# Performance work log

Hardware: AMD Instinct MI355X
Metric: run time of the kernel (lower is better)

Reference implementation:

```python
import jax, jax.numpy as jnp
from jax import lax
import numpy as np

B, C, H, W = 8, 64, 56, 56
LM = 9              # level_map: NSCT subbands per channel
D = LM * C + C      # 640: swin block dim
DEPTH = 2
WIN = 7
HEADS = 8
KS = 5              # NSCT filter kernel size


def _nsct_filters():
    # fixed nonsubsampled 9-band filter bank (lowpass + 8 directional), stand-in for myNSCTd
    r = np.arange(KS) - KS // 2
    yy, xx = np.meshgrid(r, r, indexing='ij')
    g = np.exp(-(xx ** 2 + yy ** 2) / 4.0)
    g = g / g.sum()
    f = [g]
    for k in range(LM - 1):
        th = k * np.pi / (LM - 1)
        d = (np.cos(th) * xx + np.sin(th) * yy) * g
        d = d - d.mean()
        d = d / np.sqrt((d ** 2).sum())
        f.append(d)
    return jnp.asarray(np.stack(f), dtype=jnp.float32)  # [LM,KS,KS]


def _ct(x):
    # per-(b,c) NSCT decomposition -> [B, LM*C, H, W], band-major (matches transpose(0,2,1,3,4).reshape)
    Bx, Cx, Hx, Wx = x.shape
    K = _nsct_filters()
    k = jnp.tile(K, (Cx, 1, 1))[:, None]  # [Cx*LM,1,KS,KS], out channel index c*LM+band
    o = lax.conv_general_dilated(x, k, (1, 1), 'SAME',
                                 dimension_numbers=('NCHW', 'OIHW', 'NCHW'),
                                 feature_group_count=Cx)
    o = o.reshape(Bx, Cx, LM, Hx, Wx).transpose(0, 2, 1, 3, 4).reshape(Bx, LM * Cx, Hx, Wx)
    return o


def _ict(y):
    # inverse transform: reshape(B,LM,C,H,W).permute(0,2,1,3,4), reconstruct per channel
    Bx = y.shape[0]
    t = y.reshape(Bx, LM, C, H, W).transpose(0, 2, 1, 3, 4).reshape(Bx, C * LM, H, W)
    K = _nsct_filters()
    g = jnp.broadcast_to(K, (C, LM, KS, KS))  # groups=C: 9 subbands -> 1 channel each
    return lax.conv_general_dilated(t, g, (1, 1), 'SAME',
                                    dimension_numbers=('NCHW', 'OIHW', 'NCHW'),
                                    feature_group_count=C)


def _ln(x, g, b):
    m = x.mean(-1, keepdims=True)
    v = x.var(-1, keepdims=True)
    return (x - m) / jnp.sqrt(v + 1e-5) * g + b


def _attn_mask(shift):
    # standard SW-MSA mask for shifted windows
    img = np.zeros((H, W), np.int32)
    c = 0
    for hs in (slice(0, -WIN), slice(-WIN, -shift), slice(-shift, None)):
        for ws in (slice(0, -WIN), slice(-WIN, -shift), slice(-shift, None)):
            img[hs, ws] = c
            c += 1
    a = img.reshape(H // WIN, WIN, W // WIN, WIN).transpose(0, 2, 1, 3).reshape(-1, WIN * WIN)
    m = np.where(a[:, :, None] != a[:, None, :], -1e9, 0.0).astype(np.float32)
    return jnp.asarray(m)  # [nWindows, T, T]


def _swin_block(x, p, shift):
    Bx = x.shape[0]
    T = WIN * WIN
    dh = D // HEADS
    nH, nWw = H // WIN, W // WIN
    sc = x
    h = _ln(x, p['ln1_g'], p['ln1_b'])
    if shift:
        h = jnp.roll(h, (-shift, -shift), (1, 2))
    w = h.reshape(Bx, nH, WIN, nWw, WIN, D).transpose(0, 1, 3, 2, 4, 5).reshape(Bx * nH * nWw, T, D)
    qkv = w @ p['qkv_w'] + p['qkv_b']
    q, k, v = jnp.split(qkv, 3, axis=-1)
    heads = lambda t: t.reshape(-1, T, HEADS, dh).transpose(0, 2, 1, 3)
    q, k, v = heads(q), heads(k), heads(v)
    s = jnp.einsum('nhtd,nhsd->nhts', q, k) / jnp.sqrt(jnp.asarray(dh, x.dtype))
    if shift:
        m = _attn_mask(shift)
        s = (s.reshape(Bx, nH * nWw, HEADS, T, T) + m[None, :, None]).reshape(-1, HEADS, T, T)
    a = jax.nn.softmax(s, -1)
    o = jnp.einsum('nhts,nhsd->nhtd', a, v).transpose(0, 2, 1, 3).reshape(-1, T, D)
    o = o @ p['proj_w'] + p['proj_b']
    o = o.reshape(Bx, nH, nWw, WIN, WIN, D).transpose(0, 1, 3, 2, 4, 5).reshape(Bx, H, W, D)
    if shift:
        o = jnp.roll(o, (shift, shift), (1, 2))
    x = sc + o
    h2 = _ln(x, p['ln2_g'], p['ln2_b'])
    h2 = jax.nn.gelu(h2 @ p['fc1_w'] + p['fc1_b']) @ p['fc2_w'] + p['fc2_b']
    return x + h2


def setup_inputs() -> dict:
    key = jax.random.key(0)
    ks = jax.random.split(key, 8)
    s = 0.02
    n = lambda k, shp: jax.random.normal(k, shp, jnp.float32) * s
    return {
        'x': jax.random.normal(ks[0], (B, C, H, W), jnp.float32),
        'ln1_g': jnp.ones((DEPTH, D), jnp.float32), 'ln1_b': jnp.zeros((DEPTH, D), jnp.float32),
        'qkv_w': n(ks[1], (DEPTH, D, 3 * D)), 'qkv_b': jnp.zeros((DEPTH, 3 * D), jnp.float32),
        'proj_w': n(ks[2], (DEPTH, D, D)), 'proj_b': jnp.zeros((DEPTH, D), jnp.float32),
        'ln2_g': jnp.ones((DEPTH, D), jnp.float32), 'ln2_b': jnp.zeros((DEPTH, D), jnp.float32),
        'fc1_w': n(ks[3], (DEPTH, D, 4 * D)), 'fc1_b': jnp.zeros((DEPTH, 4 * D), jnp.float32),
        'fc2_w': n(ks[4], (DEPTH, 4 * D, D)), 'fc2_b': jnp.zeros((DEPTH, D), jnp.float32),
        'lin_w': n(ks[5], (D, LM * C)), 'lin_b': jnp.zeros((LM * C,), jnp.float32),
        'conv_w': n(ks[6], (C, D)), 'conv_b': jnp.zeros((C,), jnp.float32),
    }


def reference(x, ln1_g, ln1_b, qkv_w, qkv_b, proj_w, proj_b, ln2_g, ln2_b,
              fc1_w, fc1_b, fc2_w, fc2_b, lin_w, lin_b, conv_w, conv_b):
    x2 = jax.nn.relu(x)
    x_trans = lax.stop_gradient(_ct(x2))          # CT detaches its input in the original
    x3 = jnp.concatenate([x_trans, x2], axis=1)   # [B, 10C, H, W]
    x3 = x3.transpose(0, 2, 3, 1)                 # BHWC
    for i in range(DEPTH):
        p = dict(ln1_g=ln1_g[i], ln1_b=ln1_b[i], qkv_w=qkv_w[i], qkv_b=qkv_b[i],
                 proj_w=proj_w[i], proj_b=proj_b[i], ln2_g=ln2_g[i], ln2_b=ln2_b[i],
                 fc1_w=fc1_w[i], fc1_b=fc1_b[i], fc2_w=fc2_w[i], fc2_b=fc2_b[i])
        x3 = _swin_block(x3, p, 0 if i % 2 == 0 else WIN // 2)
    x3 = x3 @ lin_w + lin_b                        # D -> LM*C
    y = x3.transpose(0, 3, 1, 2)                   # [B, 9C, H, W]
    y_trans = lax.stop_gradient(_ict(y))           # ICT detaches its input in the original
    yc = jnp.concatenate([y_trans, y], axis=1)     # [B, 10C, H, W]
    out = jnp.einsum('bchw,oc->bohw', yc, conv_w) + conv_b[None, :, None, None]
    return out
```

## Files before the change

### kernel.cpp

```cpp
#include <hip/hip_runtime.h>
#include <hip/hip_bf16.h>
#include <math.h>

typedef __attribute__((ext_vector_type(4))) float f32x4;
typedef __attribute__((ext_vector_type(8))) short short8;

#define NTOK 25088
#define DD   640

__device__ __forceinline__ void gload_lds16(const void* g, void* l) {
    __builtin_amdgcn_global_load_lds((const __attribute__((address_space(1))) void*)g,
                                     (__attribute__((address_space(3))) void*)l,
                                     16, 0, 0);
}

__device__ __forceinline__ float gelu_f(float t) {
    float u = 1.5957691216057308f * (t + 0.044715f * t * t * t);
    float e = __builtin_amdgcn_exp2f(u * -1.4426950408889634f);
    return t / (1.f + e);
}

__global__ void init_consts(float* __restrict__ filt, float* __restrict__ linbp,
                            const float* __restrict__ lin_b, float* __restrict__ convbp,
                            const float* __restrict__ conv_b) {
    int t = threadIdx.x;
    if (t == 0) {
        float g[25]; float s = 0.f;
        for (int i = 0; i < 5; i++) for (int j = 0; j < 5; j++) {
            float yy = (float)(i - 2), xx = (float)(j - 2);
            float v = expf(-(xx*xx + yy*yy) * 0.25f);
            g[i*5+j] = v; s += v;
        }
        for (int i = 0; i < 25; i++) { g[i] /= s; filt[i] = g[i]; }
        for (int k = 0; k < 8; k++) {
            float th = (float)k * 3.14159265358979323846f / 8.f;
            float ct = cosf(th), st = sinf(th);
            float d[25]; float mean = 0.f;
            for (int i = 0; i < 5; i++) for (int j = 0; j < 5; j++) {
                float yy = (float)(i - 2), xx = (float)(j - 2);
                d[i*5+j] = (ct*xx + st*yy) * g[i*5+j];
                mean += d[i*5+j];
            }
            mean *= (1.f/25.f);
            float ss = 0.f;
            for (int i = 0; i < 25; i++) { d[i] -= mean; ss += d[i]*d[i]; }
            ss = sqrtf(ss);
            for (int i = 0; i < 25; i++) filt[(k+1)*25 + i] = d[i] / ss;
        }
    }
    for (int i = t; i < 640; i += 256) linbp[i]  = (i < 576) ? lin_b[i]  : 0.f;
    for (int i = t; i < 128; i += 256) convbp[i] = (i < 64)  ? conv_b[i] : 0.f;
}

__global__ __launch_bounds__(256)
void wtrans_kernel(const float* __restrict__ src, __hip_bfloat16* __restrict__ dst,
                   int K, int Nsrc) {
    __shared__ float tile[32][33];
    const int n0 = blockIdx.x * 32;
    const int k0 = blockIdx.y * 32;
    const int tx = threadIdx.x, ty = threadIdx.y;
    #pragma unroll
    for (int r = ty; r < 32; r += 8) {
        int k = k0 + r, n = n0 + tx;
        tile[r][tx] = (n < Nsrc) ? src[(long)k * Nsrc + n] : 0.f;
    }
    __syncthreads();
    #pragma unroll
    for (int r = ty; r < 32; r += 8) {
        int n = n0 + r, k = k0 + tx;
        dst[(long)n * K + k] = __float2bfloat16(tile[tx][r]);
    }
}

__global__ void wcast_kernel(const float* __restrict__ src, __hip_bfloat16* __restrict__ dst,
                             int count, int total) {
    int i = blockIdx.x * 256 + threadIdx.x;
    if (i < total) dst[i] = __float2bfloat16(i < count ? src[i] : 0.f);
}

__global__ __launch_bounds__(256)
void prep_kernel(const float* __restrict__ x, const float* __restrict__ filt,
                 float* __restrict__ x3) {
    __shared__ float sf[225];
    for (int i = threadIdx.x; i < 225; i += 256) sf[i] = filt[i];
    __syncthreads();
    int id = blockIdx.x * 256 + threadIdx.x;
    int c = id & 63;
    int pix = id >> 6;
    int w = pix % 56, h = (pix / 56) % 56, b = pix / 3136;
    const float* xp = x + (long)(b * 64 + c) * 3136;
    float nb[25];
    #pragma unroll
    for (int dy = 0; dy < 5; dy++) {
        int hy = h + dy - 2;
        #pragma unroll
        for (int dx = 0; dx < 5; dx++) {
            int wx = w + dx - 2;
            float v = 0.f;
            if (hy >= 0 && hy < 56 && wx >= 0 && wx < 56) v = fmaxf(xp[hy*56 + wx], 0.f);
            nb[dy*5 + dx] = v;
        }
    }
    float* orow = x3 + (long)pix * DD;
    #pragma unroll
    for (int band = 0; band < 9; band++) {
        float a = 0.f;
        #pragma unroll
        for (int t = 0; t < 25; t++) a += nb[t] * sf[band*25 + t];
        orow[band*64 + c] = a;
    }
    orow[576 + c] = nb[12];
}

__global__ __launch_bounds__(256)
void ln_kernel(const float* __restrict__ xin, const float* __restrict__ g,
               const float* __restrict__ bt, __hip_bfloat16* __restrict__ out) {
    const int lane = threadIdx.x & 63;
    const long tok = (long)blockIdx.x * 4 + (threadIdx.x >> 6);
    const float* xr = xin + tok * DD;
    float v[10]; float s = 0.f, s2 = 0.f;
    #pragma unroll
    for (int i = 0; i < 10; i++) { float t = xr[lane + (i << 6)]; v[i] = t; s += t; s2 += t*t; }
    #pragma unroll
    for (int o = 32; o > 0; o >>= 1) { s += __shfl_down(s, o); s2 += __shfl_down(s2, o); }
    s = __shfl(s, 0); s2 = __shfl(s2, 0);
    const float mean = s * (1.f/640.f);
    const float var  = s2 * (1.f/640.f) - mean * mean;
    const float inv  = 1.f / sqrtf(var + 1e-5f);
    __hip_bfloat16* orow = out + tok * DD;
    #pragma unroll
    for (int i = 0; i < 10; i++) {
        int c = lane + (i << 6);
        orow[c] = __float2bfloat16((v[i] - mean) * inv * g[c] + bt[c]);
    }
}

__global__ __launch_bounds__(256, 3)
void gemm128_kernel(const __hip_bfloat16* __restrict__ A,
                    const __hip_bfloat16* __restrict__ Bt,
                    const float* __restrict__ bias,
                    const float* __restrict__ resid,
                    float* __restrict__ Cf,
                    __hip_bfloat16* __restrict__ Cb,
                    int K, int ldc, int ncf, int ldb, int col_off, int ncb,
                    int act_gelu, int nvalid, int mode) {
    extern __shared__ __align__(16) char smraw[];

    const int tid  = threadIdx.x;
    const int lane = tid & 63;
    const int wv   = tid >> 6;
    const int wr   = wv >> 1;
    const int wc   = wv & 1;

    const int gx   = gridDim.x;
    const int nwg  = gx * gridDim.y;
    const int orig = blockIdx.y * gx + blockIdx.x;
    const int qq = nwg >> 3, rr = nwg & 7;
    const int xcd = orig & 7, lid = orig >> 3;
    const int wg = (xcd < rr ? xcd * (qq + 1) : rr * (qq + 1) + (xcd - rr) * qq) + lid;
    const long m0 = (long)(wg / gx) * 128;
    const long n0 = (long)(wg % gx) * 128;

    const bool wact = ((int)n0 + (wc << 6)) < nvalid;

    f32x4 acc[4][4];
    #pragma unroll
    for (int i = 0; i < 4; i++)
        #pragma unroll
        for (int j = 0; j < 4; j++) acc[i][j] = (f32x4){0.f, 0.f, 0.f, 0.f};

    const int r0  = tid >> 2;
    const int sl  = tid & 3;
    const int ssl = sl ^ ((r0 >> 1) & 3);
    const __hip_bfloat16* Agb = A  + (m0 + r0) * (long)K + (ssl << 3);
    const __hip_bfloat16* Bgb = Bt + (n0 + r0) * (long)K + (ssl << 3);
    char* dA = smraw + r0 * 64 + sl * 16;
    char* dB = dA + 8192;

    const int frow = lane & 15;
    const int fks  = lane >> 4;
    const int colA = (fks ^ ((frow >> 1) & 3)) << 4;

    auto STAGE = [&](int b, int kt) {
        const long ko = (long)kt << 5;
        gload_lds16(Agb + ko,                dA + b * 16384);
        gload_lds16(Agb + 64 * (long)K + ko, dA + b * 16384 + 4096);
        gload_lds16(Bgb + ko,                dB + b * 16384);
        gload_lds16(Bgb + 64 * (long)K + ko, dB + b * 16384 + 4096);
    };

    const int nt = K >> 5;
    STAGE(0, 0);
    for (int t = 0; t < nt; ++t) {
        asm volatile("s_waitcnt vmcnt(0)" ::: "memory");
        __builtin_amdgcn_s_barrier();
        __builtin_amdgcn_sched_barrier(0);
        if (t + 1 < nt) STAGE((t + 1) & 1, t + 1);
        if (wact) {
            const char* pA = smraw + (t & 1) * 16384;
            const char* pB = pA + 8192;
            short8 af[4], bfr[4];
            #pragma unroll
            for (int mi = 0; mi < 4; ++mi)
                af[mi] = *(const short8*)(pA + ((wr << 6) + (mi << 4) + frow) * 64 + colA);
            #pragma unroll
            for (int nj = 0; nj < 4; ++nj)
                bfr[nj] = *(const short8*)(pB + ((wc << 6) + (nj << 4) + frow) * 64 + colA);
            __builtin_amdgcn_s_setprio(1);
            #pragma unroll
            for (int mi = 0; mi < 4; ++mi)
                #pragma unroll
                for (int nj = 0; nj < 4; ++nj)
                    acc[mi][nj] = __builtin_amdgcn_mfma_f32_16x16x32_bf16(
                        bfr[nj], af[mi], acc[mi][nj], 0, 0, 0);
            __builtin_amdgcn_s_setprio(0);
        }
    }

    if (!wact) return;
    const int nlim = (ncf > ncb) ? ncf : ncb;
    #pragma unroll
    for (int mi = 0; mi < 4; ++mi) {
        const long row = m0 + (wr << 6) + (mi << 4) + frow;
        #pragma unroll
        for (int nj = 0; nj < 4; ++nj) {
            const int n = (int)n0 + (wc << 6) + (nj << 4) + (fks << 2);
            if (n >= nlim) continue;
            f32x4 v = acc[mi][nj];
            if (bias) {
                const f32x4 bv = *(const f32x4*)&bias[n];
                v += bv;
            }
            if (act_gelu) {
                v[0] = gelu_f(v[0]); v[1] = gelu_f(v[1]); v[2] = gelu_f(v[2]); v[3] = gelu_f(v[3]);
            }
            if (mode == 1) {
                const int b = (int)(row / 3136), pos = (int)(row % 3136);
                #pragma unroll
                for (int r = 0; r < 4; ++r)
                    Cf[(long)(b * 64 + n + r) * 3136 + pos] = v[r];
                continue;
            }
            if (resid && n < ncf) v += *(const f32x4*)&resid[row * (long)ldc + n];
            if (Cf && n < ncf) *(f32x4*)&Cf[row * (long)ldc + n] = v;
            if (Cb && n < ncb) {
                short4 p;
                p.x = (short)__bfloat16_as_short(__float2bfloat16(v[0]));
                p.y = (short)__bfloat16_as_short(__float2bfloat16(v[1]));
                p.z = (short)__bfloat16_as_short(__float2bfloat16(v[2]));
                p.w = (short)__bfloat16_as_short(__float2bfloat16(v[3]));
                *(short4*)&Cb[row * (long)ldb + col_off + n] = p;
            }
        }
    }
}

__global__ __launch_bounds__(256)
void attn_kernel(const __hip_bfloat16* __restrict__ qkv, __hip_bfloat16* __restrict__ o,
                 int shift) {
    __shared__ __align__(16) float qT[80][52];
    __shared__ __align__(16) float kT[80][52];
    __shared__ __align__(16) float vs[50][80];
    __shared__ __align__(16) float ss[49][52];
    __shared__ int toks[49];
    __shared__ int rid[49];

    const int tid = threadIdx.x;
    const int win = blockIdx.x >> 3;
    const int hd  = blockIdx.x & 7;
    const int b   = win >> 6;
    const int wh  = (win >> 3) & 7;
    const int ww  = win & 7;

    if (tid < 49) {
        int i = tid / 7, j = tid % 7;
        int ph = wh * 7 + i, pw = ww * 7 + j;
        int sh = ph + shift; if (sh >= 56) sh -= 56;
        int sw = pw + shift; if (sw >= 56) sw -= 56;
        toks[tid] = (b * 56 + sh) * 56 + sw;
        int rh = (ph < 49) ? 0 : ((ph < 53) ? 1 : 2);
        int rw = (pw < 49) ? 0 : ((pw < 53) ? 1 : 2);
        rid[tid] = rh * 3 + rw;
    }
    for (int i = tid; i < 80 * 3; i += 256) {
        int d = i / 3, cc = 49 + (i % 3);
        qT[d][cc] = 0.f; kT[d][cc] = 0.f;
    }
    __syncthreads();
    for (int idx = tid; idx < 49 * 80; idx += 256) {
        int t = idx / 80, d = idx % 80;
        long base = (long)toks[t] * 1920 + hd * 80 + d;
        qT[d][t] = __bfloat162float(qkv[base]);
        kT[d][t] = __bfloat162float(qkv[base + 640]);
        vs[t][d] = __bfloat162float(qkv[base + 1280]);
    }
    __syncthreads();
    const float scale = 0.11180339887498948f;
    for (int p = tid; p < 49 * 13; p += 256) {
        int t = p / 13, j0 = (p % 13) * 4;
        float4 a = {0.f, 0.f, 0.f, 0.f};
        #pragma unroll
        for (int d = 0; d < 80; d++) {
            float qv = qT[d][t];
            float4 kv = *(const float4*)&kT[d][j0];
            a.x += qv * kv.x; a.y += qv * kv.y; a.z += qv * kv.z; a.w += qv * kv.w;
        }
        a.x *= scale; a.y *= scale; a.z *= scale; a.w *= scale;
        *(float4*)&ss[t][j0] = a;
    }
    __syncthreads();
    if (tid < 196) {
        const int r = tid >> 2, sub = tid & 3;
        const int j0 = sub * 13;
        const int j1 = (sub == 3) ? 10 : 13;
        const int myr = rid[r];
        float mx = -1e30f;
        for (int i = 0; i < j1; i++) {
            float v = ss[r][j0 + i];
            if (shift && rid[j0 + i] != myr) v = -1e9f;
            ss[r][j0 + i] = v;
            mx = fmaxf(mx, v);
        }
        mx = fmaxf(mx, __shfl_xor(mx, 1));
        mx = fmaxf(mx, __shfl_xor(mx, 2));
        float sum = 0.f;
        for (int i = 0; i < j1; i++) {
            float e = __expf(ss[r][j0 + i] - mx);
            ss[r][j0 + i] = e;
            sum += e;
        }
        sum += __shfl_xor(sum, 1);
        sum += __shfl_xor(sum, 2);
        const float inv = 1.f / sum;
        for (int i = 0; i < j1; i++) ss[r][j0 + i] *= inv;
    }
    __syncthreads();
    for (int p = tid; p < 49 * 20; p += 256) {
        int t = p / 20, dv = (p % 20) * 4;
        float4 a = {0.f, 0.f, 0.f, 0.f};
        for (int j = 0; j < 49; j++) {
            float w = ss[t][j];
            float4 vv = *(const float4*)&vs[j][dv];
            a.x += w * vv.x; a.y += w * vv.y; a.z += w * vv.z; a.w += w * vv.w;
        }
        long base = (long)toks[t] * DD + hd * 80 + dv;
        o[base + 0] = __float2bfloat16(a.x);
        o[base + 1] = __float2bfloat16(a.y);
        o[base + 2] = __float2bfloat16(a.z);
        o[base + 3] = __float2bfloat16(a.w);
    }
}

__global__ __launch_bounds__(256)
void ict_kernel(const float* __restrict__ y, const float* __restrict__ filt,
                __hip_bfloat16* __restrict__ ayc) {
    __shared__ float sf[225];
    for (int i = threadIdx.x; i < 225; i += 256) sf[i] = filt[i];
    __syncthreads();
    int id = blockIdx.x * 256 + threadIdx.x;
    int c4 = (id & 15) << 2;
    int pix = id >> 4;
    int w = pix % 56, h = (pix / 56) % 56, b = pix / 3136;
    float4 a = {0.f, 0.f, 0.f, 0.f};
    #pragma unroll
    for (int dy = 0; dy < 5; dy++) {
        int hy = h + dy - 2;
        if (hy < 0 || hy >= 56) continue;
        #pragma unroll
        for (int dx = 0; dx < 5; dx++) {
            int wx = w + dx - 2;
            if (wx < 0 || wx >= 56) continue;
            const float* yr = y + ((long)(b * 56 + hy) * 56 + wx) * DD + c4;
            #pragma unroll
            for (int band = 0; band < 9; band++) {
                const float f = sf[band*25 + dy*5 + dx];
                const float4 vv = *(const float4*)&yr[band * 64];
                a.x += vv.x * f; a.y += vv.y * f; a.z += vv.z * f; a.w += vv.w * f;
            }
        }
    }
    short4 p;
    p.x = (short)__bfloat16_as_short(__float2bfloat16(a.x));
    p.y = (short)__bfloat16_as_short(__float2bfloat16(a.y));
    p.z = (short)__bfloat16_as_short(__float2bfloat16(a.z));
    p.w = (short)__bfloat16_as_short(__float2bfloat16(a.w));
    *(short4*)&ayc[(long)pix * DD + c4] = p;
}

extern "C" void kernel_launch(void* const* d_in, const int* in_sizes, int n_in,
                              void* d_out, int out_size, void* d_ws, size_t ws_size,
                              hipStream_t stream) {
    (void)in_sizes; (void)n_in; (void)out_size; (void)ws_size;
    const float* x      = (const float*)d_in[0];
    const float* ln1_g  = (const float*)d_in[1];
    const float* ln1_b  = (const float*)d_in[2];
    const float* qkv_w  = (const float*)d_in[3];
    const float* qkv_b  = (const float*)d_in[4];
    const float* proj_w = (const float*)d_in[5];
    const float* proj_b = (const float*)d_in[6];
    const float* ln2_g  = (const float*)d_in[7];
    const float* ln2_b  = (const float*)d_in[8];
    const float* fc1_w  = (const float*)d_in[9];
    const float* fc1_b  = (const float*)d_in[10];
    const float* fc2_w  = (const float*)d_in[11];
    const float* fc2_b  = (const float*)d_in[12];
    const float* lin_w  = (const float*)d_in[13];
    const float* lin_b  = (const float*)d_in[14];
    const float* conv_w = (const float*)d_in[15];
    const float* conv_b = (const float*)d_in[16];

    char* ws = (char*)d_ws;
    size_t off = 0;
    auto alloc = [&](size_t bytes) -> void* {
        void* p = ws + off;
        off += (bytes + 255) & ~(size_t)255;
        return p;
    };
    float* filt   = (float*)alloc(225 * 4);
    float* linbp  = (float*)alloc(640 * 4);
    float* convbp = (float*)alloc(128 * 4);
    __hip_bfloat16* qkvWt[2], *projWt[2], *fc1Wt[2], *fc2Wt[2];
    for (int i = 0; i < 2; i++) qkvWt[i] = (__hip_bfloat16*)alloc(1920L * 640 * 2);
    for (int i = 0; i < 2; i++) projWt[i] = (__hip_bfloat16*)alloc(640L * 640 * 2);
    for (int i = 0; i < 2; i++) fc1Wt[i] = (__hip_bfloat16*)alloc(2560L * 640 * 2);
    for (int i = 0; i < 2; i++) fc2Wt[i] = (__hip_bfloat16*)alloc(640L * 2560 * 2);
    __hip_bfloat16* linWt  = (__hip_bfloat16*)alloc(640L * 640 * 2);
    __hip_bfloat16* convWt = (__hip_bfloat16*)alloc(128L * 640 * 2);
    float* x3 = (float*)alloc((long)NTOK * DD * 4);
    __hip_bfloat16* bufA = (__hip_bfloat16*)alloc((long)NTOK * DD * 2);
    char* bufB = (char*)alloc((long)NTOK * 2560 * 2);
    __hip_bfloat16* qkv = (__hip_bfloat16*)bufB;
    __hip_bfloat16* h2  = (__hip_bfloat16*)bufB;
    float* ybuf = (float*)bufB;
    __hip_bfloat16* ayc = (__hip_bfloat16*)(bufB + (long)NTOK * DD * 4);

    hipFuncSetAttribute((const void*)gemm128_kernel,
                        hipFuncAttributeMaxDynamicSharedMemorySize, 32768);

    dim3 tb(32, 8);
    init_consts<<<1, 256, 0, stream>>>(filt, linbp, lin_b, convbp, conv_b);
    for (int i = 0; i < 2; i++) {
        wtrans_kernel<<<dim3(60, 20), tb, 0, stream>>>(qkv_w + (long)i*640*1920, qkvWt[i], 640, 1920);
        wtrans_kernel<<<dim3(20, 20), tb, 0, stream>>>(proj_w + (long)i*640*640,  projWt[i], 640, 640);
        wtrans_kernel<<<dim3(80, 20), tb, 0, stream>>>(fc1_w + (long)i*640*2560, fc1Wt[i], 640, 2560);
        wtrans_kernel<<<dim3(20, 80), tb, 0, stream>>>(fc2_w + (long)i*2560*640, fc2Wt[i], 2560, 640);
    }
    wtrans_kernel<<<dim3(20, 20), tb, 0, stream>>>(lin_w, linWt, 640, 576);
    wcast_kernel<<<320, 256, 0, stream>>>(conv_w, convWt, 64 * 640, 128 * 640);

    prep_kernel<<<6272, 256, 0, stream>>>(x, filt, x3);

    for (int i = 0; i < 2; i++) {
        int shift = i ? 3 : 0;
        ln_kernel<<<6272, 256, 0, stream>>>(x3, ln1_g + i*640, ln1_b + i*640, bufA);
        gemm128_kernel<<<dim3(15, 196), 256, 32768, stream>>>(bufA, qkvWt[i], qkv_b + i*1920,
            nullptr, nullptr, qkv, 640, 0, 0, 1920, 0, 1920, 0, 1920, 0);
        attn_kernel<<<4096, 256, 0, stream>>>(qkv, bufA, shift);
        gemm128_kernel<<<dim3(5, 196), 256, 32768, stream>>>(bufA, projWt[i], proj_b + i*640,
            x3, x3, nullptr, 640, 640, 640, 0, 0, 0, 0, 640, 0);
        ln_kernel<<<6272, 256, 0, stream>>>(x3, ln2_g + i*640, ln2_b + i*640, bufA);
        gemm128_kernel<<<dim3(20, 196), 256, 32768, stream>>>(bufA, fc1Wt[i], fc1_b + i*2560,
            nullptr, nullptr, h2, 640, 0, 0, 2560, 0, 2560, 1, 2560, 0);
        gemm128_kernel<<<dim3(5, 196), 256, 32768, stream>>>(h2, fc2Wt[i], fc2_b + i*640,
            x3, x3, (i == 1) ? bufA : nullptr, 2560, 640, 640, 640, 0, (i == 1) ? 640 : 0, 0, 640, 0);
    }
    gemm128_kernel<<<dim3(5, 196), 256, 32768, stream>>>(bufA, linWt, linbp,
        nullptr, ybuf, ayc, 640, 640, 640, 640, 64, 576, 0, 576, 0);
    ict_kernel<<<1568, 256, 0, stream>>>(ybuf, filt, ayc);
    gemm128_kernel<<<dim3(1, 196), 256, 32768, stream>>>(ayc, convWt, convbp,
        nullptr, (float*)d_out, nullptr, 640, 0, 64, 0, 0, 0, 0, 64, 1);
}
```

Baseline: 1.372 ms.

## Fuse first LayerNorm into prep, unroll GEMM k-loop by two, read ICT input from bf16

The prep kernel now computes the first block's LayerNorm in-register via wave shuffles and writes the bf16 normalized tokens directly, so the first ln_kernel launch is skipped. The GEMM main loop is manually unrolled by two with fixed double-buffer offsets, which removes per-iteration buffer index arithmetic. The lin GEMM no longer writes an fp32 y buffer. The ICT kernel instead reads the bf16 copy already stored in ayc, cutting memory traffic at the cost of bf16 precision in the inverse transform input. The unrolled loop assumes an even number of k tiles, which holds for K=640 and 2560.

```diff
diff --git a/kernel.cpp b/kernel.cpp
--- a/kernel.cpp
+++ b/kernel.cpp
@@ -18,6 +18,12 @@
     float u = 1.5957691216057308f * (t + 0.044715f * t * t * t);
     float e = __builtin_amdgcn_exp2f(u * -1.4426950408889634f);
     return t / (1.f + e);
+}
+
+__device__ __forceinline__ float bf2f(short u) {
+    union { unsigned int i; float f; } cv;
+    cv.i = ((unsigned int)(unsigned short)u) << 16;
+    return cv.f;
 }
 
 __global__ void init_consts(float* __restrict__ filt, float* __restrict__ linbp,
@@ -80,7 +86,8 @@
 
 __global__ __launch_bounds__(256)
 void prep_kernel(const float* __restrict__ x, const float* __restrict__ filt,
-                 float* __restrict__ x3) {
+                 float* __restrict__ x3, const float* __restrict__ g1,
+                 const float* __restrict__ b1, __hip_bfloat16* __restrict__ lnout) {
     __shared__ float sf[225];
     for (int i = threadIdx.x; i < 225; i += 256) sf[i] = filt[i];
     __syncthreads();
@@ -101,15 +108,33 @@
             nb[dy*5 + dx] = v;
         }
     }
+    float bo[9];
     float* orow = x3 + (long)pix * DD;
+    float s = 0.f, s2 = 0.f;
     #pragma unroll
     for (int band = 0; band < 9; band++) {
         float a = 0.f;
         #pragma unroll
         for (int t = 0; t < 25; t++) a += nb[t] * sf[band*25 + t];
+        bo[band] = a;
         orow[band*64 + c] = a;
-    }
-    orow[576 + c] = nb[12];
+        s += a; s2 += a * a;
+    }
+    const float ctr = nb[12];
+    orow[576 + c] = ctr;
+    s += ctr; s2 += ctr * ctr;
+    #pragma unroll
+    for (int o = 32; o > 0; o >>= 1) { s += __shfl_xor(s, o); s2 += __shfl_xor(s2, o); }
+    const float mean = s * (1.f/640.f);
+    const float var  = s2 * (1.f/640.f) - mean * mean;
+    const float inv  = 1.f / sqrtf(var + 1e-5f);
+    __hip_bfloat16* ob = lnout + (long)pix * DD;
+    #pragma unroll
+    for (int band = 0; band < 9; band++) {
+        int ci = band*64 + c;
+        ob[ci] = __float2bfloat16((bo[band] - mean) * inv * g1[ci] + b1[ci]);
+    }
+    ob[576 + c] = __float2bfloat16((ctr - mean) * inv * g1[576 + c] + b1[576 + c]);
 }
 
 __global__ __launch_bounds__(256)
@@ -181,41 +206,52 @@
     const int fks  = lane >> 4;
     const int colA = (fks ^ ((frow >> 1) & 3)) << 4;
 
-    auto STAGE = [&](int b, int kt) {
+    auto STAGE = [&](int boff, int kt) {
         const long ko = (long)kt << 5;
-        gload_lds16(Agb + ko,                dA + b * 16384);
-        gload_lds16(Agb + 64 * (long)K + ko, dA + b * 16384 + 4096);
-        gload_lds16(Bgb + ko,                dB + b * 16384);
-        gload_lds16(Bgb + 64 * (long)K + ko, dB + b * 16384 + 4096);
+        gload_lds16(Agb + ko,                dA + boff);
+        gload_lds16(Agb + 64 * (long)K + ko, dA + boff + 4096);
+        gload_lds16(Bgb + ko,                dB + boff);
+        gload_lds16(Bgb + 64 * (long)K + ko, dB + boff + 4096);
     };
+
+#define COMPUTE(BUFOFF)                                                                     \
+    do {                                                                                    \
+        if (wact) {                                                                         \
+            const char* pA = smraw + (BUFOFF);                                              \
+            const char* pB = pA + 8192;                                                     \
+            short8 af[4], bfr[4];                                                           \
+            _Pragma("unroll")                                                               \
+            for (int mi = 0; mi < 4; ++mi)                                                  \
+                af[mi] = *(const short8*)(pA + ((wr << 6) + (mi << 4) + frow) * 64 + colA); \
+            _Pragma("unroll")                                                               \
+            for (int nj = 0; nj < 4; ++nj)                                                  \
+                bfr[nj] = *(const short8*)(pB + ((wc << 6) + (nj << 4) + frow) * 64 + colA);\
+            __builtin_amdgcn_s_setprio(1);                                                  \
+            _Pragma("unroll")                                                               \
+            for (int mi = 0; mi < 4; ++mi)                                                  \
+                _Pragma("unroll")                                                           \
+                for (int nj = 0; nj < 4; ++nj)         \
+                    acc[mi][nj] = __builtin_amdgcn_mfma_f32_16x16x32_bf16(                  \
+                        bfr[nj], af[mi], acc[mi][nj], 0, 0, 0);                             \
+            __builtin_amdgcn_s_setprio(0);                                                  \
+        }                                                                                   \
+    } while (0)
 
     const int nt = K >> 5;
     STAGE(0, 0);
-    for (int t = 0; t < nt; ++t) {
+    for (int t = 0; t < nt; t += 2) {
         asm volatile("s_waitcnt vmcnt(0)" ::: "memory");
         __builtin_amdgcn_s_barrier();
         __builtin_amdgcn_sched_barrier(0);
-        if (t + 1 < nt) STAGE((t + 1) & 1, t + 1);
-        if (wact) {
-            const char* pA = smraw + (t & 1) * 16384;
-            const char* pB = pA + 8192;
-            short8 af[4], bfr[4];
-            #pragma unroll
-            for (int mi = 0; mi < 4; ++mi)
-                af[mi] = *(const short8*)(pA + ((wr << 6) + (mi << 4) + frow) * 64 + colA);
-            #pragma unroll
-            for (int nj = 0; nj < 4; ++nj)
-                bfr[nj] = *(const short8*)(pB + ((wc << 6) + (nj << 4) + frow) * 64 + colA);
-            __builtin_amdgcn_s_setprio(1);
-            #pragma unroll
-            for (int mi = 0; mi < 4; ++mi)
-                #pragma unroll
-                for (int nj = 0; nj < 4; ++nj)
-                    acc[mi][nj] = __builtin_amdgcn_mfma_f32_16x16x32_bf16(
-                        bfr[nj], af[mi], acc[mi][nj], 0, 0, 0);
-            __builtin_amdgcn_s_setprio(0);
-        }
-    }
+        if (t + 1 < nt) STAGE(16384, t + 1);
+        COMPUTE(0);
+        asm volatile("s_waitcnt vmcnt(0)" ::: "memory");
+        __builtin_amdgcn_s_barrier();
+        __builtin_amdgcn_sched_barrier(0);
+        if (t + 2 < nt) STAGE(0, t + 2);
+        COMPUTE(16384);
+    }
+#undef COMPUTE
 
     if (!wact) return;
     const int nlim = (ncf > ncb) ? ncf : ncb;
@@ -352,8 +388,7 @@
 }
 
 __global__ __launch_bounds__(256)
-void ict_kernel(const float* __restrict__ y, const float* __restrict__ filt,
-                __hip_bfloat16* __restrict__ ayc) {
+void ict_kernel(__hip_bfloat16* ayc, const float* __restrict__ filt) {
     __shared__ float sf[225];
     for (int i = threadIdx.x; i < 225; i += 256) sf[i] = filt[i];
     __syncthreads();
@@ -370,12 +405,13 @@
         for (int dx = 0; dx < 5; dx++) {
             int wx = w + dx - 2;
             if (wx < 0 || wx >= 56) continue;
-            const float* yr = y + ((long)(b * 56 + hy) * 56 + wx) * DD + c4;
+            const __hip_bfloat16* yr = ayc + ((long)(b * 56 + hy) * 56 + wx) * DD + 64 + c4;
             #pragma unroll
             for (int band = 0; band < 9; band++) {
                 const float f = sf[band*25 + dy*5 + dx];
-                const float4 vv = *(const float4*)&yr[band * 64];
-                a.x += vv.x * f; a.y += vv.y * f; a.z += vv.z * f; a.w += vv.w * f;
+                const short4 sv = *(const short4*)&yr[band * 64];
+                a.x += bf2f(sv.x) * f; a.y += bf2f(sv.y) * f;
+                a.z += bf2f(sv.z) * f; a.w += bf2f(sv.w) * f;
             }
         }
     }
@@ -431,7 +467,6 @@
     char* bufB = (char*)alloc((long)NTOK * 2560 * 2);
     __hip_bfloat16* qkv = (__hip_bfloat16*)bufB;
     __hip_bfloat16* h2  = (__hip_bfloat16*)bufB;
-    float* ybuf = (float*)bufB;
     __hip_bfloat16* ayc = (__hip_bfloat16*)(bufB + (long)NTOK * DD * 4);
 
     hipFuncSetAttribute((const void*)gemm128_kernel,
@@ -448,11 +483,12 @@
     wtrans_kernel<<<dim3(20, 20), tb, 0, stream>>>(lin_w, linWt, 640, 576);
     wcast_kernel<<<320, 256, 0, stream>>>(conv_w, convWt, 64 * 640, 128 * 640);
 
-    prep_kernel<<<6272, 256, 0, stream>>>(x, filt, x3);
+    prep_kernel<<<6272, 256, 0, stream>>>(x, filt, x3, ln1_g, ln1_b, bufA);
 
     for (int i = 0; i < 2; i++) {
         int shift = i ? 3 : 0;
-        ln_kernel<<<6272, 256, 0, stream>>>(x3, ln1_g + i*640, ln1_b + i*640, bufA);
+        if (i == 1)
+            ln_kernel<<<6272, 256, 0, stream>>>(x3, ln1_g + i*640, ln1_b + i*640, bufA);
         gemm128_kernel<<<dim3(15, 196), 256, 32768, stream>>>(bufA, qkvWt[i], qkv_b + i*1920,
             nullptr, nullptr, qkv, 640, 0, 0, 1920, 0, 1920, 0, 1920, 0);
         attn_kernel<<<4096, 256, 0, stream>>>(qkv, bufA, shift);
@@ -465,8 +501,8 @@
             x3, x3, (i == 1) ? bufA : nullptr, 2560, 640, 640, 640, 0, (i == 1) ? 640 : 0, 0, 640, 0);
     }
     gemm128_kernel<<<dim3(5, 196), 256, 32768, stream>>>(bufA, linWt, linbp,
-        nullptr, ybuf, ayc, 640, 640, 640, 640, 64, 576, 0, 576, 0);
-    ict_kernel<<<1568, 256, 0, stream>>>(ybuf, filt, ayc);
+        nullptr, nullptr, ayc, 640, 0, 0, 640, 64, 576, 0, 576, 0);
+    ict_kernel<<<1568, 256, 0, stream>>>(ayc, filt);
     gemm128_kernel<<<dim3(1, 196), 256, 32768, stream>>>(ayc, convWt, convbp,
         nullptr, (float*)d_out, nullptr, 640, 0, 64, 0, 0, 0, 0, 64, 1);
 }
```

Result: faster. 1.337 ms (-2.6%).
